# Optimization experiments

Hardware: AMD Instinct MI355X
Metric: run time of the kernel (lower is better)

## Reference

```python
import jax, jax.numpy as jnp
import numpy as np

EPS = 1e-4  # Moller-Trumbore epsilon from the original

def _dot(a, b):
    return jnp.sum(a * b, axis=-1)

def setup_inputs() -> dict:
    key = jax.random.key(0)
    k1, k2, k3 = jax.random.split(key, 3)
    N, V, F = 2048, 2500, 4096
    p = jax.random.normal(k1, (N, 3), dtype=jnp.float32)
    v = jax.random.normal(k2, (V, 3), dtype=jnp.float32)
    f = jax.random.randint(k3, (F, 3), 0, V, dtype=jnp.int64)
    return {"p": p, "v": v, "f": f}

def reference(p, v, f):
    N = p.shape[0]
    faces = v[f]                      # (F,3,3)
    a, b, c = faces[:, 0], faces[:, 1], faces[:, 2]   # (F,3) each
    pe = p[None]                      # (1,N,3), broadcasts against (F,1,3)

    # --- point-to-triangle distance = min over the 3 edge segments (matches original output math) ---
    e1 = a - b                        # faces[:,0]-faces[:,1]
    e2 = c - b
    e3 = c - a

    def seg(e, ref_pt, q0, q1):
        # s = ((ref_pt - p) . e) / |e|^2, clamped; closest = s*q0 + (1-s)*q1  (original formula kept verbatim)
        m2 = _dot(e, e)[:, None]                       # (F,1)
        s = jnp.clip(_dot(ref_pt[:, None] - pe, e[:, None]) / m2, 0.0, 1.0)[..., None]  # (F,N,1)
        cl = s * q0[:, None] + (1.0 - s) * q1[:, None]  # (F,N,3)
        d = jnp.linalg.norm(cl - pe, axis=-1)           # (F,N)
        return d, cl

    d12, c12 = seg(e1, a, b, a)   # s12 from (p0-p).e1; closest = s*p1+(1-s)*p0
    d23, c23 = seg(e2, c, b, c)   # s23 from (p2-p).e2; closest = s*p1+(1-s)*p2
    d31, c31 = seg(e3, c, a, c)   # s31 from (p2-p).e3; closest = s*p0+(1-s)*p2

    d_all = jnp.stack([d12, d23, d31], axis=0)          # (3,F,N)
    c_all = jnp.stack([c12, c23, c31], axis=0)          # (3,F,N,3)
    which = jnp.argmin(d_all, axis=0)                   # (F,N)
    dist = jnp.min(d_all, axis=0)                       # (F,N)
    closest = jnp.take_along_axis(c_all, which[None, ..., None], axis=0)[0]  # (F,N,3)

    # nearest face per query point
    fidx = jnp.argmin(jnp.abs(dist), axis=0)            # (N,)
    dmin = jnp.take_along_axis(dist, fidx[None], axis=0)  # (1,N)
    closest_p = closest[fidx, jnp.arange(N)]            # (N,3)

    # --- Moller-Trumbore ray-triangle parity test toward mesh centroid ---
    dirv = v.mean(axis=0)[None] - p                     # (N,3)
    me1 = b - a                                         # faces[:,1]-faces[:,0]
    me2 = c - a
    pvec = jnp.cross(dirv[None], me2[:, None])          # (F,N,3)
    det = _dot(me1[:, None], pvec)                      # (F,N)
    tvec = pe - a[:, None]                              # (F,N,3)
    u = _dot(tvec, pvec) / det
    qvec = jnp.cross(tvec, me1[:, None])                # (F,N,3)
    dd = _dot(dirv[None], qvec) / det
    t = _dot(me2[:, None], qvec) / det
    hit = (jnp.abs(det) > EPS) & (u >= 0) & (u <= 1) & (dd >= 0) & (u + dd <= 1) & (t > EPS)
    counts = jnp.sum(hit, axis=0)                       # (N,)
    inside = (0.5 - (counts % 2 == 1).astype(dmin.dtype)) * 2.0  # +1 outside, -1 inside

    dmin = dmin * inside[None]                          # (1,N)
    return (dmin, closest_p)
```

## Files before the change

### kernel.cpp

```cpp
#include <hip/hip_runtime.h>
#include <math.h>

#define TRI_EPS 1e-4f

__global__ __launch_bounds__(256) void prep_kernel(
    const float* __restrict__ v, const int* __restrict__ f,
    float4* __restrict__ fdat, float* __restrict__ vm, int V, int F) {
    const int t = threadIdx.x;
    const int j = blockIdx.x * 256 + t;
    if (j < F) {
        const int i0 = f[3 * j + 0];
        const int i1 = f[3 * j + 1];
        const int i2 = f[3 * j + 2];
        const float ax = v[3 * i0 + 0], ay = v[3 * i0 + 1], az = v[3 * i0 + 2];
        const float bx = v[3 * i1 + 0], by = v[3 * i1 + 1], bz = v[3 * i1 + 2];
        const float cx = v[3 * i2 + 0], cy = v[3 * i2 + 1], cz = v[3 * i2 + 2];
        const float e1x = ax - bx, e1y = ay - by, e1z = az - bz;
        const float e2x = cx - bx, e2y = cy - by, e2z = cz - bz;
        const float e3x = cx - ax, e3y = cy - ay, e3z = cz - az;
        const float m1 = e1x * e1x + e1y * e1y + e1z * e1z;
        const float m2 = e2x * e2x + e2y * e2y + e2z * e2z;
        const float m3 = e3x * e3x + e3y * e3y + e3z * e3z;
        fdat[3 * j + 0] = make_float4(ax, ay, az, 1.f / m1);
        fdat[3 * j + 1] = make_float4(bx, by, bz, 1.f / m2);
        fdat[3 * j + 2] = make_float4(cx, cy, cz, 1.f / m3);
    }
    if (blockIdx.x == 0) {
        __shared__ float sx[256], sy[256], sz[256];
        float x = 0.f, y = 0.f, z = 0.f;
        for (int i = t; i < V; i += 256) {
            x += v[3 * i + 0];
            y += v[3 * i + 1];
            z += v[3 * i + 2];
        }
        sx[t] = x; sy[t] = y; sz[t] = z;
        __syncthreads();
        for (int off = 128; off > 0; off >>= 1) {
            if (t < off) {
                sx[t] += sx[t + off];
                sy[t] += sy[t + off];
                sz[t] += sz[t + off];
            }
            __syncthreads();
        }
        if (t == 0) {
            vm[0] = sx[0] / (float)V;
            vm[1] = sy[0] / (float)V;
            vm[2] = sz[0] / (float)V;
        }
    }
}

struct FP {
    float d1, d2, d3;
    float x1, y1, z1, x2, y2, z2, x3, y3, z3;
    float apx, apy, apz;
};

__device__ __forceinline__ FP face_point(
    const float4 ra, const float4 rb, const float4 rc,
    const float e1x, const float e1y, const float e1z,
    const float e2x, const float e2y, const float e2z,
    const float e3x, const float e3y, const float e3z,
    const float px, const float py, const float pz) {
    FP r;
    const float ax = ra.x, ay = ra.y, az = ra.z;
    const float bx = rb.x, by = rb.y, bz = rb.z;
    const float cx = rc.x, cy = rc.y, cz = rc.z;
    r.apx = ax - px; r.apy = ay - py; r.apz = az - pz;
    const float cpx = cx - px, cpy = cy - py, cpz = cz - pz;

    float s1 = (r.apx * e1x + r.apy * e1y + r.apz * e1z) * ra.w;
    s1 = fminf(fmaxf(s1, 0.f), 1.f);
    const float o1 = 1.f - s1;
    r.x1 = s1 * bx + o1 * ax;
    r.y1 = s1 * by + o1 * ay;
    r.z1 = s1 * bz + o1 * az;
    float ux = r.x1 - px, uy = r.y1 - py, uz = r.z1 - pz;
    r.d1 = ux * ux + uy * uy + uz * uz;

    float s2 = (cpx * e2x + cpy * e2y + cpz * e2z) * rb.w;
    s2 = fminf(fmaxf(s2, 0.f), 1.f);
    const float o2 = 1.f - s2;
    r.x2 = s2 * bx + o2 * cx;
    r.y2 = s2 * by + o2 * cy;
    r.z2 = s2 * bz + o2 * cz;
    ux = r.x2 - px; uy = r.y2 - py; uz = r.z2 - pz;
    r.d2 = ux * ux + uy * uy + uz * uz;

    float s3 = (cpx * e3x + cpy * e3y + cpz * e3z) * rc.w;
    s3 = fminf(fmaxf(s3, 0.f), 1.f);
    const float o3 = 1.f - s3;
    r.x3 = s3 * ax + o3 * cx;
    r.y3 = s3 * ay + o3 * cy;
    r.z3 = s3 * az + o3 * cz;
    ux = r.x3 - px; uy = r.y3 - py; uz = r.z3 - pz;
    r.d3 = ux * ux + uy * uy + uz * uz;
    return r;
}

__device__ __forceinline__ void pair_update(
    const float4 ra, const float4 rb, const float4 rc,
    const float e1x, const float e1y, const float e1z,
    const float e2x, const float e2y, const float e2z,
    const float e3x, const float e3y, const float e3z,
    const float px, const float py, const float pz,
    const float dx, const float dy, const float dz, const int j,
    float& bd2, int& bid, int& hits) {
    const FP r = face_point(ra, rb, rc, e1x, e1y, e1z, e2x, e2y, e2z,
                            e3x, e3y, e3z, px, py, pz);
    float fd2 = r.d1; int eid = 0;
    if (r.d2 < fd2) { fd2 = r.d2; eid = 1; }
    if (r.d3 < fd2) { fd2 = r.d3; eid = 2; }
    if (fd2 < bd2) { bd2 = fd2; bid = (j << 2) | eid; }

    const float pvx = dy * e3z - dz * e3y;
    const float pvy = dz * e3x - dx * e3z;
    const float pvz = dx * e3y - dy * e3x;
    const float det = -(e1x * pvx + e1y * pvy + e1z * pvz);
    const float tu = -(r.apx * pvx + r.apy * pvy + r.apz * pvz);
    const float qvx = r.apy * e1z - r.apz * e1y;
    const float qvy = r.apz * e1x - r.apx * e1z;
    const float qvz = r.apx * e1y - r.apy * e1x;
    const float td = dx * qvx + dy * qvy + dz * qvz;
    const float tn = e3x * qvx + e3y * qvy + e3z * qvz;
    const float adet = fabsf(det);
    const float sd = (det > 0.f) ? 1.f : -1.f;
    const float su = tu * sd;
    const float sq = td * sd;
    const float st = tn * sd;
    if (adet > TRI_EPS && su >= 0.f && su <= adet && sq >= 0.f &&
        (su + sq) <= adet && st > TRI_EPS * adet)
        hits++;
}

__global__ __launch_bounds__(256) void sdf_main(
    const float* __restrict__ p, const float4* __restrict__ fd,
    const float* __restrict__ vm, float* __restrict__ out, int N, int F) {
    const int t = threadIdx.x;
    const int i0 = blockIdx.x * 2;
    const int i1 = i0 + 1;
    const bool has1 = (i1 < N);

    const float vmx = vm[0], vmy = vm[1], vmz = vm[2];
    const float p0x = p[3 * i0 + 0], p0y = p[3 * i0 + 1], p0z = p[3 * i0 + 2];
    const float p1x = has1 ? p[3 * i1 + 0] : 0.f;
    const float p1y = has1 ? p[3 * i1 + 1] : 0.f;
    const float p1z = has1 ? p[3 * i1 + 2] : 0.f;
    const float d0x = vmx - p0x, d0y = vmy - p0y, d0z = vmz - p0z;
    const float d1x = vmx - p1x, d1y = vmy - p1y, d1z = vmz - p1z;

    float Ad2 = INFINITY; int Aid = 0x7fffffff; int Ah = 0;
    float Bd2 = INFINITY; int Bid = 0x7fffffff; int Bh = 0;

    int j = t;
    bool valid = (j < F);
    float4 ra, rb, rc;
    if (valid) {
        ra = fd[3 * j + 0];
        rb = fd[3 * j + 1];
        rc = fd[3 * j + 2];
    }
    while (valid) {
        const int jn = j + 256;
        const bool vn = (jn < F);
        float4 na, nb, nc;
        if (vn) {
            na = fd[3 * jn + 0];
            nb = fd[3 * jn + 1];
            nc = fd[3 * jn + 2];
        }
        const float e1x = ra.x - rb.x, e1y = ra.y - rb.y, e1z = ra.z - rb.z;
        const float e2x = rc.x - rb.x, e2y = rc.y - rb.y, e2z = rc.z - rb.z;
        const float e3x = rc.x - ra.x, e3y = rc.y - ra.y, e3z = rc.z - ra.z;

        pair_update(ra, rb, rc, e1x, e1y, e1z, e2x, e2y, e2z, e3x, e3y, e3z,
                    p0x, p0y, p0z, d0x, d0y, d0z, j, Ad2, Aid, Ah);
        pair_update(ra, rb, rc, e1x, e1y, e1z, e2x, e2y, e2z, e3x, e3y, e3z,
                    p1x, p1y, p1z, d1x, d1y, d1z, j, Bd2, Bid, Bh);

        j = jn; valid = vn;
        ra = na; rb = nb; rc = nc;
    }

    __shared__ float sd2[2][256];
    __shared__ int sid[2][256];
    __shared__ int shh[2][256];
    sd2[0][t] = Ad2; sid[0][t] = Aid; shh[0][t] = Ah;
    sd2[1][t] = Bd2; sid[1][t] = Bid; shh[1][t] = Bh;
    __syncthreads();
    for (int off = 128; off > 0; off >>= 1) {
        if (t < off) {
            #pragma unroll
            for (int q = 0; q < 2; q++) {
                const float dov = sd2[q][t + off];
                const int iov = sid[q][t + off];
                if (dov < sd2[q][t] || (dov == sd2[q][t] && iov < sid[q][t])) {
                    sd2[q][t] = dov;
                    sid[q][t] = iov;
                }
                shh[q][t] += shh[q][t + off];
            }
        }
        __syncthreads();
    }

    if (t < 2) {
        const int i = i0 + t;
        if (i < N) {
            const float px = t ? p1x : p0x;
            const float py = t ? p1y : p0y;
            const float pz = t ? p1z : p0z;
            const int bid = sid[t][0];
            const int jw = bid >> 2;
            const int eid = bid & 3;
            const float4 wa = fd[3 * jw + 0];
            const float4 wb = fd[3 * jw + 1];
            const float4 wc = fd[3 * jw + 2];
            const float e1x = wa.x - wb.x, e1y = wa.y - wb.y, e1z = wa.z - wb.z;
            const float e2x = wc.x - wb.x, e2y = wc.y - wb.y, e2z = wc.z - wb.z;
            const float e3x = wc.x - wa.x, e3y = wc.y - wa.y, e3z = wc.z - wa.z;
            const FP r = face_point(wa, wb, wc, e1x, e1y, e1z, e2x, e2y, e2z,
                                    e3x, e3y, e3z, px, py, pz);
            float clx = r.x1, cly = r.y1, clz = r.z1;
            if (eid == 1) { clx = r.x2; cly = r.y2; clz = r.z2; }
            if (eid == 2) { clx = r.x3; cly = r.y3; clz = r.z3; }
            const float d = sqrtf(sd2[t][0]);
            out[i] = (shh[t][0] & 1) ? -d : d;
            out[N + 3 * i + 0] = clx;
            out[N + 3 * i + 1] = cly;
            out[N + 3 * i + 2] = clz;
        }
    }
}

extern "C" void kernel_launch(void* const* d_in, const int* in_sizes, int n_in,
                              void* d_out, int out_size, void* d_ws,
                              size_t ws_size, hipStream_t stream) {
    const float* p = (const float*)d_in[0];
    const float* v = (const float*)d_in[1];
    const int* f = (const int*)d_in[2];
    float* out = (float*)d_out;
    float* ws = (float*)d_ws;

    const int N = in_sizes[0] / 3;
    const int V = in_sizes[1] / 3;
    const int F = in_sizes[2] / 3;

    float4* fdat = (float4*)((char*)d_ws + 16);

    prep_kernel<<<(F + 255) / 256, 256, 0, stream>>>(v, f, fdat, ws, V, F);
    sdf_main<<<(N + 1) / 2, 256, 0, stream>>>(p, fdat, ws, out, N, F);
}
```

Before: 42.73 us.

## Split faces across blocks, one thread per point, with separate reduction kernel

```diff
diff --git a/kernel.cpp b/kernel.cpp
--- a/kernel.cpp
+++ b/kernel.cpp
@@ -21,9 +21,12 @@
         const float m1 = e1x * e1x + e1y * e1y + e1z * e1z;
         const float m2 = e2x * e2x + e2y * e2y + e2z * e2z;
         const float m3 = e3x * e3x + e3y * e3y + e3z * e3z;
-        fdat[3 * j + 0] = make_float4(ax, ay, az, 1.f / m1);
-        fdat[3 * j + 1] = make_float4(bx, by, bz, 1.f / m2);
-        fdat[3 * j + 2] = make_float4(cx, cy, cz, 1.f / m3);
+        fdat[6 * j + 0] = make_float4(ax, ay, az, 1.f / m1);
+        fdat[6 * j + 1] = make_float4(bx, by, bz, 1.f / m2);
+        fdat[6 * j + 2] = make_float4(cx, cy, cz, 1.f / m3);
+        fdat[6 * j + 3] = make_float4(e1x, e1y, e1z, 0.f);
+        fdat[6 * j + 4] = make_float4(e2x, e2y, e2z, 0.f);
+        fdat[6 * j + 5] = make_float4(e3x, e3y, e3z, 0.f);
     }
     if (blockIdx.x == 0) {
         __shared__ float sx[256], sy[256], sz[256];
@@ -136,101 +139,103 @@
 
 __global__ __launch_bounds__(256) void sdf_main(
     const float* __restrict__ p, const float4* __restrict__ fd,
-    const float* __restrict__ vm, float* __restrict__ out, int N, int F) {
+    const float* __restrict__ vm,
+    float* __restrict__ D2, int* __restrict__ ID, int* __restrict__ H,
+    int N, int F, int C, int CS) {
+    const int k = blockIdx.x % C;
+    const int pg = blockIdx.x / C;
+    const int i = pg * 256 + threadIdx.x;
+    if (i >= N) return;
+
+    const float px = p[3 * i + 0];
+    const float py = p[3 * i + 1];
+    const float pz = p[3 * i + 2];
+    const float dx = vm[0] - px;
+    const float dy = vm[1] - py;
+    const float dz = vm[2] - pz;
+
+    float bd2 = INFINITY;
+    int bid = 0x7fffffff;
+    int hits = 0;
+
+    const int j0 = k * CS;
+    const int j1 = min(F, j0 + CS);
+    #pragma unroll 4
+    for (int j = j0; j < j1; ++j) {
+        const float4 ra  = fd[6 * j + 0];
+        const float4 rb  = fd[6 * j + 1];
+        const float4 rc  = fd[6 * j + 2];
+        const float4 re1 = fd[6 * j + 3];
+        const float4 re2 = fd[6 * j + 4];
+        const float4 re3 = fd[6 * j + 5];
+        pair_update(ra, rb, rc, re1.x, re1.y, re1.z, re2.x, re2.y, re2.z,
+                    re3.x, re3.y, re3.z, px, py, pz, dx, dy, dz, j,
+                    bd2, bid, hits);
+    }
+    const int o = k * N + i;
+    D2[o] = bd2;
+    ID[o] = bid;
+    H[o] = hits;
+}
+
+__global__ __launch_bounds__(256) void sdf_reduce(
+    const float* __restrict__ p, const float4* __restrict__ fd,
+    const float* __restrict__ D2, const int* __restrict__ ID,
+    const int* __restrict__ H, float* __restrict__ out, int N, int C) {
     const int t = threadIdx.x;
-    const int i0 = blockIdx.x * 2;
-    const int i1 = i0 + 1;
-    const bool has1 = (i1 < N);
-
-    const float vmx = vm[0], vmy = vm[1], vmz = vm[2];
-    const float p0x = p[3 * i0 + 0], p0y = p[3 * i0 + 1], p0z = p[3 * i0 + 2];
-    const float p1x = has1 ? p[3 * i1 + 0] : 0.f;
-    const float p1y = has1 ? p[3 * i1 + 1] : 0.f;
-    const float p1z = has1 ? p[3 * i1 + 2] : 0.f;
-    const float d0x = vmx - p0x, d0y = vmy - p0y, d0z = vmz - p0z;
-    const float d1x = vmx - p1x, d1y = vmy - p1y, d1z = vmz - p1z;
-
-    float Ad2 = INFINITY; int Aid = 0x7fffffff; int Ah = 0;
-    float Bd2 = INFINITY; int Bid = 0x7fffffff; int Bh = 0;
-
-    int j = t;
-    bool valid = (j < F);
-    float4 ra, rb, rc;
-    if (valid) {
-        ra = fd[3 * j + 0];
-        rb = fd[3 * j + 1];
-        rc = fd[3 * j + 2];
-    }
-    while (valid) {
-        const int jn = j + 256;
-        const bool vn = (jn < F);
-        float4 na, nb, nc;
-        if (vn) {
-            na = fd[3 * jn + 0];
-            nb = fd[3 * jn + 1];
-            nc = fd[3 * jn + 2];
-        }
-        const float e1x = ra.x - rb.x, e1y = ra.y - rb.y, e1z = ra.z - rb.z;
-        const float e2x = rc.x - rb.x, e2y = rc.y - rb.y, e2z = rc.z - rb.z;
-        const float e3x = rc.x - ra.x, e3y = rc.y - ra.y, e3z = rc.z - ra.z;
-
-        pair_update(ra, rb, rc, e1x, e1y, e1z, e2x, e2y, e2z, e3x, e3y, e3z,
-                    p0x, p0y, p0z, d0x, d0y, d0z, j, Ad2, Aid, Ah);
-        pair_update(ra, rb, rc, e1x, e1y, e1z, e2x, e2y, e2z, e3x, e3y, e3z,
-                    p1x, p1y, p1z, d1x, d1y, d1z, j, Bd2, Bid, Bh);
-
-        j = jn; valid = vn;
-        ra = na; rb = nb; rc = nc;
-    }
-
-    __shared__ float sd2[2][256];
-    __shared__ int sid[2][256];
-    __shared__ int shh[2][256];
-    sd2[0][t] = Ad2; sid[0][t] = Aid; shh[0][t] = Ah;
-    sd2[1][t] = Bd2; sid[1][t] = Bid; shh[1][t] = Bh;
+    const int q = t & 63;
+    const int c = t >> 6;
+    const int i = blockIdx.x * 64 + q;
+
+    float bd2 = INFINITY;
+    int bid = 0x7fffffff;
+    int hits = 0;
+    if (i < N) {
+        for (int k = c; k < C; k += 4) {
+            const int o = k * N + i;
+            const float d = D2[o];
+            const int id = ID[o];
+            if (d < bd2 || (d == bd2 && id < bid)) { bd2 = d; bid = id; }
+            hits += H[o];
+        }
+    }
+    __shared__ float ld2[4][64];
+    __shared__ int lid[4][64];
+    __shared__ int lh[4][64];
+    ld2[c][q] = bd2;
+    lid[c][q] = bid;
+    lh[c][q] = hits;
     __syncthreads();
-    for (int off = 128; off > 0; off >>= 1) {
-        if (t < off) {
-            #pragma unroll
-            for (int q = 0; q < 2; q++) {
-                const float dov = sd2[q][t + off];
-                const int iov = sid[q][t + off];
-                if (dov < sd2[q][t] || (dov == sd2[q][t] && iov < sid[q][t])) {
-                    sd2[q][t] = dov;
-                    sid[q][t] = iov;
-                }
-                shh[q][t] += shh[q][t + off];
-            }
-        }
-        __syncthreads();
-    }
-
-    if (t < 2) {
-        const int i = i0 + t;
-        if (i < N) {
-            const float px = t ? p1x : p0x;
-            const float py = t ? p1y : p0y;
-            const float pz = t ? p1z : p0z;
-            const int bid = sid[t][0];
-            const int jw = bid >> 2;
-            const int eid = bid & 3;
-            const float4 wa = fd[3 * jw + 0];
-            const float4 wb = fd[3 * jw + 1];
-            const float4 wc = fd[3 * jw + 2];
-            const float e1x = wa.x - wb.x, e1y = wa.y - wb.y, e1z = wa.z - wb.z;
-            const float e2x = wc.x - wb.x, e2y = wc.y - wb.y, e2z = wc.z - wb.z;
-            const float e3x = wc.x - wa.x, e3y = wc.y - wa.y, e3z = wc.z - wa.z;
-            const FP r = face_point(wa, wb, wc, e1x, e1y, e1z, e2x, e2y, e2z,
-                                    e3x, e3y, e3z, px, py, pz);
-            float clx = r.x1, cly = r.y1, clz = r.z1;
-            if (eid == 1) { clx = r.x2; cly = r.y2; clz = r.z2; }
-            if (eid == 2) { clx = r.x3; cly = r.y3; clz = r.z3; }
-            const float d = sqrtf(sd2[t][0]);
-            out[i] = (shh[t][0] & 1) ? -d : d;
-            out[N + 3 * i + 0] = clx;
-            out[N + 3 * i + 1] = cly;
-            out[N + 3 * i + 2] = clz;
-        }
+    if (t < 64 && i < N) {
+        #pragma unroll
+        for (int cc = 1; cc < 4; cc++) {
+            const float d = ld2[cc][q];
+            const int id = lid[cc][q];
+            if (d < bd2 || (d == bd2 && id < bid)) { bd2 = d; bid = id; }
+            hits += lh[cc][q];
+        }
+        const float px = p[3 * i + 0];
+        const float py = p[3 * i + 1];
+        const float pz = p[3 * i + 2];
+        const int jw = bid >> 2;
+        const int eid = bid & 3;
+        const float4 wa  = fd[6 * jw + 0];
+        const float4 wb  = fd[6 * jw + 1];
+        const float4 wc  = fd[6 * jw + 2];
+        const float4 we1 = fd[6 * jw + 3];
+        const float4 we2 = fd[6 * jw + 4];
+        const float4 we3 = fd[6 * jw + 5];
+        const FP r = face_point(wa, wb, wc, we1.x, we1.y, we1.z,
+                                we2.x, we2.y, we2.z, we3.x, we3.y, we3.z,
+                                px, py, pz);
+        float clx = r.x1, cly = r.y1, clz = r.z1;
+        if (eid == 1) { clx = r.x2; cly = r.y2; clz = r.z2; }
+        if (eid == 2) { clx = r.x3; cly = r.y3; clz = r.z3; }
+        const float d = sqrtf(bd2);
+        out[i] = (hits & 1) ? -d : d;
+        out[N + 3 * i + 0] = clx;
+        out[N + 3 * i + 1] = cly;
+        out[N + 3 * i + 2] = clz;
     }
 }
 
@@ -241,14 +246,28 @@
     const float* v = (const float*)d_in[1];
     const int* f = (const int*)d_in[2];
     float* out = (float*)d_out;
-    float* ws = (float*)d_ws;
+    float* vm = (float*)d_ws;
 
     const int N = in_sizes[0] / 3;
     const int V = in_sizes[1] / 3;
     const int F = in_sizes[2] / 3;
 
+    const size_t fdat_bytes = (size_t)F * 6 * sizeof(float4);
     float4* fdat = (float4*)((char*)d_ws + 16);
-
-    prep_kernel<<<(F + 255) / 256, 256, 0, stream>>>(v, f, fdat, ws, V, F);
-    sdf_main<<<(N + 1) / 2, 256, 0, stream>>>(p, fdat, ws, out, N, F);
-}
+    char* pbase = (char*)d_ws + 16 + fdat_bytes;
+
+    int C = 256;
+    while (C > 8 &&
+           16 + fdat_bytes + 3ull * C * N * 4ull > ws_size)
+        C >>= 1;
+    const int CS = (F + C - 1) / C;
+
+    float* D2 = (float*)pbase;
+    int* ID = (int*)(pbase + 1ull * C * N * 4ull);
+    int* H = (int*)(pbase + 2ull * C * N * 4ull);
+
+    const int npg = (N + 255) / 256;
+    prep_kernel<<<(F + 255) / 256, 256, 0, stream>>>(v, f, fdat, vm, V, F);
+    sdf_main<<<npg * C, 256, 0, stream>>>(p, fdat, vm, D2, ID, H, N, F, C, CS);
+    sdf_reduce<<<(N + 63) / 64, 256, 0, stream>>>(p, fdat, D2, ID, H, out, N, C);
+}
```

Result: slower. 82.09 us (+92.1%).
